# Kernel optimization log

Hardware: AMD Instinct MI355X
Metric: run time of the kernel (lower is better)

## Reference

```python
import jax, jax.numpy as jnp
import numpy as np

LN_EPS = 1e-5


def setup_inputs() -> dict:
    key = jax.random.key(0)
    ks = jax.random.split(key, 8)
    N, c_z, H, C = 256, 128, 4, 32
    s = 0.02  # small init scale for stable softmax
    return {
        "z": jax.random.normal(ks[0], (N, N, c_z), dtype=jnp.float32),
        "ln_g": jnp.ones((c_z,), jnp.float32),
        "ln_b": jnp.zeros((c_z,), jnp.float32),
        "Wb": jax.random.normal(ks[1], (c_z, H), dtype=jnp.float32) * s,
        "Wq": jax.random.normal(ks[2], (c_z, H, C), dtype=jnp.float32) * s,
        "Wk": jax.random.normal(ks[3], (c_z, H, C), dtype=jnp.float32) * s,
        "Wv": jax.random.normal(ks[4], (c_z, H, C), dtype=jnp.float32) * s,
        "Wg": jax.random.normal(ks[5], (c_z, H, C), dtype=jnp.float32) * s,
        "bg": jnp.ones((H, C), jnp.float32),
        "Wo": jax.random.normal(ks[6], (H, C, c_z), dtype=jnp.float32) * s,
        "bo": jnp.zeros((c_z,), jnp.float32),
    }


def reference(z, ln_g, ln_b, Wb, Wq, Wk, Wv, Wg, bg, Wo, bo):
    # TriangleAttention, node_type='starting_node' (Algorithm 13).
    # z: (N, N, c_z)
    C = Wq.shape[-1]
    # LayerNorm over c_z
    mu = jnp.mean(z, axis=-1, keepdims=True)
    var = jnp.var(z, axis=-1, keepdims=True)
    x = (z - mu) * jax.lax.rsqrt(var + LN_EPS) * ln_g + ln_b
    # pairwise additive bias: b[h, j, k] = (x @ Wb)[j, k, h]
    b = jnp.einsum('jkz,zh->hjk', x, Wb)
    # per-head projections; attention over second residue axis (-2),
    # first residue axis i acts as batch
    q = jnp.einsum('ijz,zhc->ijhc', x, Wq)
    k = jnp.einsum('ijz,zhc->ijhc', x, Wk)
    v = jnp.einsum('ijz,zhc->ijhc', x, Wv)
    scores = jnp.einsum('iqhc,ikhc->hiqk', q, k) / jnp.sqrt(jnp.asarray(C, x.dtype))
    scores = scores + b[:, None, :, :]  # broadcast bias over batch axis i
    a = jax.nn.softmax(scores, axis=-1)  # (h, i, q, k)
    o = jnp.einsum('hiqk,ikhc->iqhc', a, v)
    g = jax.nn.sigmoid(jnp.einsum('ijz,zhc->ijhc', x, Wg) + bg)
    o = o * g
    out = jnp.einsum('iqhc,hcz->iqz', o, Wo) + bo
    return out
```

## Files before the change

kernel.cpp:

```cpp
#include <hip/hip_runtime.h>
#include <hip/hip_bf16.h>
#include <math.h>


#define NN 256
#define CZ 128

typedef __attribute__((ext_vector_type(8))) short bf16x8;
typedef __attribute__((ext_vector_type(4))) float f32x4;

__device__ __forceinline__ f32x4 mfma16(bf16x8 a, bf16x8 b, f32x4 c) {
  return __builtin_amdgcn_mfma_f32_16x16x32_bf16(a, b, c, 0, 0, 0);
}
__device__ __forceinline__ unsigned short f2bf(float f) {
  unsigned b = __float_as_uint(f);
  return (unsigned short)((b + 0x7FFFu + ((b >> 16) & 1u)) >> 16);
}

__global__ __launch_bounds__(128) void k_prep(const float* __restrict__ Wq, const float* __restrict__ Wk,
                                              const float* __restrict__ Wv, const float* __restrict__ Wg,
                                              const float* __restrict__ Wo, unsigned short* __restrict__ Wt) {
  int n = blockIdx.x, t = threadIdx.x;
  const float* srcs[5] = {Wq, Wk, Wv, Wg, Wo};
  float v = srcs[n >> 7][t * 128 + (n & 127)];
  Wt[n * 128 + t] = f2bf(v);
}

__global__ __launch_bounds__(256) void k_ln(const float* __restrict__ z,
                                            const float* __restrict__ ln_g,
                                            const float* __restrict__ ln_b,
                                            const float* __restrict__ Wb,
                                            unsigned short* __restrict__ xb,
                                            float* __restrict__ bT) {
  int wave = threadIdx.x >> 6, lane = threadIdx.x & 63;
  int pos = blockIdx.x * 4 + wave;
  float2 v = ((const float2*)(z + (size_t)pos * CZ))[lane];
  float s = v.x + v.y, sq = v.x * v.x + v.y * v.y;
#pragma unroll
  for (int o = 1; o < 64; o <<= 1) { s += __shfl_xor(s, o); sq += __shfl_xor(sq, o); }
  float mean = s * (1.0f / CZ);
  float var = sq * (1.0f / CZ) - mean * mean;
  float rstd = rsqrtf(var + 1e-5f);
  int c0 = lane * 2;
  float x0 = (v.x - mean) * rstd * ln_g[c0] + ln_b[c0];
  float x1 = (v.y - mean) * rstd * ln_g[c0 + 1] + ln_b[c0 + 1];
  unsigned pk = (unsigned)f2bf(x0) | ((unsigned)f2bf(x1) << 16);
  ((unsigned*)(xb + (size_t)pos * CZ))[lane] = pk;
  float4 w0 = *(const float4*)(Wb + c0 * 4);
  float4 w1 = *(const float4*)(Wb + (c0 + 1) * 4);
  float b0 = x0 * w0.x + x1 * w1.x;
  float b1 = x0 * w0.y + x1 * w1.y;
  float b2 = x0 * w0.z + x1 * w1.z;
  float b3 = x0 * w0.w + x1 * w1.w;
#pragma unroll
  for (int o = 1; o < 64; o <<= 1) {
    b0 += __shfl_xor(b0, o); b1 += __shfl_xor(b1, o);
    b2 += __shfl_xor(b2, o); b3 += __shfl_xor(b3, o);
  }
  if (lane == 0) {
    int j = pos >> 8, kk = pos & 255;
    bT[0 * 65536 + kk * 256 + j] = b0;
    bT[1 * 65536 + kk * 256 + j] = b1;
    bT[2 * 65536 + kk * 256 + j] = b2;
    bT[3 * 65536 + kk * 256 + j] = b3;
  }
}

__global__ __launch_bounds__(512, 1) void k_fused(const unsigned short* __restrict__ xb,
                                                  const unsigned short* __restrict__ Wt,
                                                  const float* __restrict__ bT,
                                                  const float* __restrict__ bg,
                                                  const float* __restrict__ bo,
                                                  float* __restrict__ out) {
  __shared__ unsigned short ks[256][40];
  __shared__ unsigned short vt[32][264];
  __shared__ unsigned short qs[8][32][40];
  int i = blockIdx.x;
  int t = threadIdx.x, w = t >> 6, lane = t & 63, l16 = lane & 15, g = lane >> 4;
  int rbase = w * 32;
  const float sc = 0.17677669529663687f;

  bf16x8 xa[2][4];
#pragma unroll
  for (int m = 0; m < 2; m++)
#pragma unroll
    for (int kt = 0; kt < 4; kt++)
      xa[m][kt] = *(const bf16x8*)(xb + (size_t)(i * 256 + rbase + m * 16 + l16) * CZ + kt * 32 + g * 8);

  f32x4 oac[2][8];
#pragma unroll
  for (int m = 0; m < 2; m++)
#pragma unroll
    for (int n = 0; n < 8; n++) oac[m][n] = (f32x4){0.f, 0.f, 0.f, 0.f};

  for (int h = 0; h < 4; h++) {
    __syncthreads();
    f32x4 d[2][2];
#pragma unroll
    for (int m = 0; m < 2; m++)
#pragma unroll
      for (int n = 0; n < 2; n++) d[m][n] = (f32x4){0.f, 0.f, 0.f, 0.f};
#pragma unroll
    for (int kt = 0; kt < 4; kt++)
#pragma unroll
      for (int n = 0; n < 2; n++) {
        bf16x8 b = *(const bf16x8*)(Wt + (size_t)(128 + h * 32 + n * 16 + l16) * CZ + kt * 32 + g * 8);
#pragma unroll
        for (int m = 0; m < 2; m++) d[m][n] = mfma16(xa[m][kt], b, d[m][n]);
      }
#pragma unroll
    for (int m = 0; m < 2; m++)
#pragma unroll
      for (int n = 0; n < 2; n++)
#pragma unroll
        for (int r = 0; r < 4; r++) ks[rbase + m * 16 + g * 4 + r][n * 16 + l16] = f2bf(d[m][n][r]);
#pragma unroll
    for (int m = 0; m < 2; m++)
#pragma unroll
      for (int n = 0; n < 2; n++) d[m][n] = (f32x4){0.f, 0.f, 0.f, 0.f};
#pragma unroll
    for (int kt = 0; kt < 4; kt++)
#pragma unroll
      for (int n = 0; n < 2; n++) {
        bf16x8 b = *(const bf16x8*)(Wt + (size_t)(256 + h * 32 + n * 16 + l16) * CZ + kt * 32 + g * 8);
#pragma unroll
        for (int m = 0; m < 2; m++) d[m][n] = mfma16(xa[m][kt], b, d[m][n]);
      }
#pragma unroll
    for (int m = 0; m < 2; m++)
#pragma unroll
      for (int n = 0; n < 2; n++) {
        ushort4 pk;
        pk.x = f2bf(d[m][n][0]); pk.y = f2bf(d[m][n][1]);
        pk.z = f2bf(d[m][n][2]); pk.w = f2bf(d[m][n][3]);
        *(ushort4*)&vt[n * 16 + l16][rbase + m * 16 + g * 4] = pk;
      }
#pragma unroll
    for (int m = 0; m < 2; m++)
#pragma unroll
      for (int n = 0; n < 2; n++) d[m][n] = (f32x4){0.f, 0.f, 0.f, 0.f};
#pragma unroll
    for (int kt = 0; kt < 4; kt++)
#pragma unroll
      for (int n = 0; n < 2; n++) {
        bf16x8 b = *(const bf16x8*)(Wt + (size_t)(0 + h * 32 + n * 16 + l16) * CZ + kt * 32 + g * 8);
#pragma unroll
        for (int m = 0; m < 2; m++) d[m][n] = mfma16(xa[m][kt], b, d[m][n]);
      }
#pragma unroll
    for (int m = 0; m < 2; m++)
#pragma unroll
      for (int n = 0; n < 2; n++)
#pragma unroll
        for (int r = 0; r < 4; r++) qs[w][m * 16 + g * 4 + r][n * 16 + l16] = f2bf(d[m][n][r]);
#pragma unroll
    for (int m = 0; m < 2; m++)
#pragma unroll
      for (int n = 0; n < 2; n++) d[m][n] = (f32x4){0.f, 0.f, 0.f, 0.f};
#pragma unroll
    for (int kt = 0; kt < 4; kt++)
#pragma unroll
      for (int n = 0; n < 2; n++) {
        bf16x8 b = *(const bf16x8*)(Wt + (size_t)(384 + h * 32 + n * 16 + l16) * CZ + kt * 32 + g * 8);
#pragma unroll
        for (int m = 0; m < 2; m++) d[m][n] = mfma16(xa[m][kt], b, d[m][n]);
      }
    float gt[2][2][4];
    float bgv0 = bg[h * 32 + l16], bgv1 = bg[h * 32 + 16 + l16];
#pragma unroll
    for (int m = 0; m < 2; m++)
#pragma unroll
      for (int n = 0; n < 2; n++)
#pragma unroll
        for (int r = 0; r < 4; r++)
          gt[m][n][r] = 1.0f / (1.0f + __expf(-(d[m][n][r] + (n ? bgv1 : bgv0))));
    __syncthreads();

    bf16x8 qa[2];
#pragma unroll
    for (int m = 0; m < 2; m++) qa[m] = *(const bf16x8*)&qs[w][m * 16 + l16][g * 8];
    f32x4 oat[2][2], lsum[2];
#pragma unroll
    for (int m = 0; m < 2; m++) {
      lsum[m] = (f32x4){0.f, 0.f, 0.f, 0.f};
#pragma unroll
      for (int n = 0; n < 2; n++) oat[m][n] = (f32x4){0.f, 0.f, 0.f, 0.f};
    }
    const float* bb = bT + (size_t)h * 65536;
    for (int kc = 0; kc < 8; kc++) {
      bf16x8 kb[2];
#pragma unroll
      for (int n = 0; n < 2; n++) kb[n] = *(const bf16x8*)&ks[kc * 32 + n * 16 + l16][g * 8];
      f32x4 p[2][2];
#pragma unroll
      for (int m = 0; m < 2; m++)
#pragma unroll
        for (int n = 0; n < 2; n++) {
          f32x4 s = mfma16(qa[m], kb[n], (f32x4){0.f, 0.f, 0.f, 0.f});
          float4 bv = *(const float4*)(bb + (size_t)(kc * 32 + n * 16 + l16) * 256 + rbase + m * 16 + g * 4);
          p[m][n][0] = __expf(s[0] * sc + bv.x);
          p[m][n][1] = __expf(s[1] * sc + bv.y);
          p[m][n][2] = __expf(s[2] * sc + bv.z);
          p[m][n][3] = __expf(s[3] * sc + bv.w);
          lsum[m] += p[m][n];
        }
#pragma unroll
      for (int m = 0; m < 2; m++)
#pragma unroll
        for (int n = 0; n < 2; n++)
#pragma unroll
          for (int r = 0; r < 4; r++) qs[w][m * 16 + g * 4 + r][n * 16 + l16] = f2bf(p[m][n][r]);
      bf16x8 pa[2], vb[2];
#pragma unroll
      for (int m = 0; m < 2; m++) pa[m] = *(const bf16x8*)&qs[w][m * 16 + l16][g * 8];
#pragma unroll
      for (int n = 0; n < 2; n++) vb[n] = *(const bf16x8*)&vt[n * 16 + l16][kc * 32 + g * 8];
#pragma unroll
      for (int m = 0; m < 2; m++)
#pragma unroll
        for (int n = 0; n < 2; n++) oat[m][n] = mfma16(pa[m], vb[n], oat[m][n]);
    }
#pragma unroll
    for (int m = 0; m < 2; m++)
#pragma unroll
      for (int off = 1; off < 16; off <<= 1)
#pragma unroll
        for (int r = 0; r < 4; r++) lsum[m][r] += __shfl_xor(lsum[m][r], off);
#pragma unroll
    for (int m = 0; m < 2; m++) {
      f32x4 inv;
#pragma unroll
      for (int r = 0; r < 4; r++) inv[r] = 1.0f / lsum[m][r];
#pragma unroll
      for (int n = 0; n < 2; n++)
#pragma unroll
        for (int r = 0; r < 4; r++)
          qs[w][m * 16 + g * 4 + r][n * 16 + l16] = f2bf(oat[m][n][r] * inv[r] * gt[m][n][r]);
    }
    bf16x8 pa2[2];
#pragma unroll
    for (int m = 0; m < 2; m++) pa2[m] = *(const bf16x8*)&qs[w][m * 16 + l16][g * 8];
#pragma unroll
    for (int n2 = 0; n2 < 8; n2++) {
      bf16x8 wb = *(const bf16x8*)(Wt + (size_t)(512 + n2 * 16 + l16) * CZ + h * 32 + g * 8);
#pragma unroll
      for (int m = 0; m < 2; m++) oac[m][n2] = mfma16(pa2[m], wb, oac[m][n2]);
    }
  }
#pragma unroll
  for (int n2 = 0; n2 < 8; n2++) {
    int zc = n2 * 16 + l16;
    float bv = bo[zc];
#pragma unroll
    for (int m = 0; m < 2; m++)
#pragma unroll
      for (int r = 0; r < 4; r++)
        out[(size_t)(i * 256 + rbase + m * 16 + g * 4 + r) * 128 + zc] = oac[m][n2][r] + bv;
  }
}

extern "C" void kernel_launch(void* const* d_in, const int* in_sizes, int n_in,
                              void* d_out, int out_size, void* d_ws, size_t ws_size,
                              hipStream_t stream) {
  const float* z    = (const float*)d_in[0];
  const float* ln_g = (const float*)d_in[1];
  const float* ln_b = (const float*)d_in[2];
  const float* Wb   = (const float*)d_in[3];
  const float* Wq   = (const float*)d_in[4];
  const float* Wk   = (const float*)d_in[5];
  const float* Wv   = (const float*)d_in[6];
  const float* Wg   = (const float*)d_in[7];
  const float* bg   = (const float*)d_in[8];
  const float* Wo   = (const float*)d_in[9];
  const float* bo   = (const float*)d_in[10];
  float* out = (float*)d_out;

  char* ws = (char*)d_ws;
  unsigned short* xb = (unsigned short*)(ws + 0);
  float*          bT = (float*)(ws + 16777216);
  unsigned short* Wt = (unsigned short*)(ws + 17825792);

  k_prep<<<640, 128, 0, stream>>>(Wq, Wk, Wv, Wg, Wo, Wt);
  k_ln<<<16384, 256, 0, stream>>>(z, ln_g, ln_b, Wb, xb, bT);
  k_fused<<<256, 512, 0, stream>>>(xb, Wt, bT, bg, bo, out);
}
```

Before: 217.1 us.

## Split fused attention into per-head blocks plus a separate output-projection GEMM

The single fused kernel (one 512-thread block per batch row, looping over 4 heads) is replaced by a per-(row, head) kernel with 256 threads and higher occupancy. Each warp now handles 64 query rows. The gated attention output is written to a bf16 workspace, and a separate k_out GEMM kernel applies Wo and bo. This exposes 4x more blocks to fill the GPU and removes the per-head barrier loop. The cost is an extra global round trip of the gated output, an extra launch, and redundant reads of xb per head.

Measured after the change: 223.2 us. 1.03x slower.

```diff
diff --git a/kernel.cpp b/kernel.cpp
--- a/kernel.cpp
+++ b/kernel.cpp
@@ -66,42 +66,37 @@
   }
 }
 
-__global__ __launch_bounds__(512, 1) void k_fused(const unsigned short* __restrict__ xb,
-                                                  const unsigned short* __restrict__ Wt,
-                                                  const float* __restrict__ bT,
-                                                  const float* __restrict__ bg,
-                                                  const float* __restrict__ bo,
-                                                  float* __restrict__ out) {
+__global__ __launch_bounds__(256, 3) void k_head(const unsigned short* __restrict__ xb,
+                                                 const unsigned short* __restrict__ Wt,
+                                                 const float* __restrict__ bT,
+                                                 const float* __restrict__ bg,
+                                                 unsigned short* __restrict__ og) {
   __shared__ unsigned short ks[256][40];
   __shared__ unsigned short vt[32][264];
-  __shared__ unsigned short qs[8][32][40];
-  int i = blockIdx.x;
+  __shared__ unsigned short qs[4][32][40];
+  int i = blockIdx.x, h = blockIdx.y;
   int t = threadIdx.x, w = t >> 6, lane = t & 63, l16 = lane & 15, g = lane >> 4;
-  int rbase = w * 32;
   const float sc = 0.17677669529663687f;
 
-  bf16x8 xa[2][4];
-#pragma unroll
-  for (int m = 0; m < 2; m++)
+  bf16x8 qa[2][2];
+  f32x4 gt[2][2][2];
+
+#pragma unroll
+  for (int rh = 0; rh < 2; rh++) {
+    int r0 = w * 64 + rh * 32;
+    bf16x8 xa[2][4];
+#pragma unroll
+    for (int m = 0; m < 2; m++)
+#pragma unroll
+      for (int kt = 0; kt < 4; kt++)
+        xa[m][kt] = *(const bf16x8*)(xb + (size_t)(i * 256 + r0 + m * 16 + l16) * CZ + kt * 32 + g * 8);
+    f32x4 d[2][2];
+#pragma unroll
+    for (int m = 0; m < 2; m++)
+#pragma unroll
+      for (int n = 0; n < 2; n++) d[m][n] = (f32x4){0.f, 0.f, 0.f, 0.f};
 #pragma unroll
     for (int kt = 0; kt < 4; kt++)
-      xa[m][kt] = *(const bf16x8*)(xb + (size_t)(i * 256 + rbase + m * 16 + l16) * CZ + kt * 32 + g * 8);
-
-  f32x4 oac[2][8];
-#pragma unroll
-  for (int m = 0; m < 2; m++)
-#pragma unroll
-    for (int n = 0; n < 8; n++) oac[m][n] = (f32x4){0.f, 0.f, 0.f, 0.f};
-
-  for (int h = 0; h < 4; h++) {
-    __syncthreads();
-    f32x4 d[2][2];
-#pragma unroll
-    for (int m = 0; m < 2; m++)
-#pragma unroll
-      for (int n = 0; n < 2; n++) d[m][n] = (f32x4){0.f, 0.f, 0.f, 0.f};
-#pragma unroll
-    for (int kt = 0; kt < 4; kt++)
 #pragma unroll
       for (int n = 0; n < 2; n++) {
         bf16x8 b = *(const bf16x8*)(Wt + (size_t)(128 + h * 32 + n * 16 + l16) * CZ + kt * 32 + g * 8);
@@ -113,7 +108,7 @@
 #pragma unroll
       for (int n = 0; n < 2; n++)
 #pragma unroll
-        for (int r = 0; r < 4; r++) ks[rbase + m * 16 + g * 4 + r][n * 16 + l16] = f2bf(d[m][n][r]);
+        for (int r = 0; r < 4; r++) ks[r0 + m * 16 + g * 4 + r][n * 16 + l16] = f2bf(d[m][n][r]);
 #pragma unroll
     for (int m = 0; m < 2; m++)
 #pragma unroll
@@ -133,7 +128,7 @@
         ushort4 pk;
         pk.x = f2bf(d[m][n][0]); pk.y = f2bf(d[m][n][1]);
         pk.z = f2bf(d[m][n][2]); pk.w = f2bf(d[m][n][3]);
-        *(ushort4*)&vt[n * 16 + l16][rbase + m * 16 + g * 4] = pk;
+        *(ushort4*)&vt[n * 16 + l16][r0 + m * 16 + g * 4] = pk;
       }
 #pragma unroll
     for (int m = 0; m < 2; m++)
@@ -154,6 +149,8 @@
 #pragma unroll
         for (int r = 0; r < 4; r++) qs[w][m * 16 + g * 4 + r][n * 16 + l16] = f2bf(d[m][n][r]);
 #pragma unroll
+    for (int m = 0; m < 2; m++) qa[rh][m] = *(const bf16x8*)&qs[w][m * 16 + l16][g * 8];
+#pragma unroll
     for (int m = 0; m < 2; m++)
 #pragma unroll
       for (int n = 0; n < 2; n++) d[m][n] = (f32x4){0.f, 0.f, 0.f, 0.f};
@@ -165,7 +162,6 @@
 #pragma unroll
         for (int m = 0; m < 2; m++) d[m][n] = mfma16(xa[m][kt], b, d[m][n]);
       }
-    float gt[2][2][4];
     float bgv0 = bg[h * 32 + l16], bgv1 = bg[h * 32 + 16 + l16];
 #pragma unroll
     for (int m = 0; m < 2; m++)
@@ -173,12 +169,14 @@
       for (int n = 0; n < 2; n++)
 #pragma unroll
         for (int r = 0; r < 4; r++)
-          gt[m][n][r] = 1.0f / (1.0f + __expf(-(d[m][n][r] + (n ? bgv1 : bgv0))));
-    __syncthreads();
-
-    bf16x8 qa[2];
-#pragma unroll
-    for (int m = 0; m < 2; m++) qa[m] = *(const bf16x8*)&qs[w][m * 16 + l16][g * 8];
+          gt[rh][m][n][r] = 1.0f / (1.0f + __expf(-(d[m][n][r] + (n ? bgv1 : bgv0))));
+  }
+  __syncthreads();
+
+  const float* bb = bT + (size_t)h * 65536;
+#pragma unroll
+  for (int qh = 0; qh < 2; qh++) {
+    int rq = w * 64 + qh * 32;
     f32x4 oat[2][2], lsum[2];
 #pragma unroll
     for (int m = 0; m < 2; m++) {
@@ -186,7 +184,6 @@
 #pragma unroll
       for (int n = 0; n < 2; n++) oat[m][n] = (f32x4){0.f, 0.f, 0.f, 0.f};
     }
-    const float* bb = bT + (size_t)h * 65536;
     for (int kc = 0; kc < 8; kc++) {
       bf16x8 kb[2];
 #pragma unroll
@@ -196,8 +193,8 @@
       for (int m = 0; m < 2; m++)
 #pragma unroll
         for (int n = 0; n < 2; n++) {
-          f32x4 s = mfma16(qa[m], kb[n], (f32x4){0.f, 0.f, 0.f, 0.f});
-          float4 bv = *(const float4*)(bb + (size_t)(kc * 32 + n * 16 + l16) * 256 + rbase + m * 16 + g * 4);
+          f32x4 s = mfma16(qa[qh][m], kb[n], (f32x4){0.f, 0.f, 0.f, 0.f});
+          float4 bv = *(const float4*)(bb + (size_t)(kc * 32 + n * 16 + l16) * 256 + rq + m * 16 + g * 4);
           p[m][n][0] = __expf(s[0] * sc + bv.x);
           p[m][n][1] = __expf(s[1] * sc + bv.y);
           p[m][n][2] = __expf(s[2] * sc + bv.z);
@@ -235,27 +232,54 @@
       for (int n = 0; n < 2; n++)
 #pragma unroll
         for (int r = 0; r < 4; r++)
-          qs[w][m * 16 + g * 4 + r][n * 16 + l16] = f2bf(oat[m][n][r] * inv[r] * gt[m][n][r]);
-    }
-    bf16x8 pa2[2];
-#pragma unroll
-    for (int m = 0; m < 2; m++) pa2[m] = *(const bf16x8*)&qs[w][m * 16 + l16][g * 8];
-#pragma unroll
-    for (int n2 = 0; n2 < 8; n2++) {
-      bf16x8 wb = *(const bf16x8*)(Wt + (size_t)(512 + n2 * 16 + l16) * CZ + h * 32 + g * 8);
-#pragma unroll
-      for (int m = 0; m < 2; m++) oac[m][n2] = mfma16(pa2[m], wb, oac[m][n2]);
-    }
-  }
-#pragma unroll
-  for (int n2 = 0; n2 < 8; n2++) {
-    int zc = n2 * 16 + l16;
+          qs[w][m * 16 + g * 4 + r][n * 16 + l16] = f2bf(oat[m][n][r] * inv[r] * gt[qh][m][n][r]);
+    }
+#pragma unroll
+    for (int e = 0; e < 4; e++) {
+      int idx = e * 64 + lane;
+      int row = idx >> 3, c4 = (idx & 7) * 4;
+      *(ushort4*)(og + (size_t)(i * 256 + rq + row) * 128 + h * 32 + c4) = *(ushort4*)&qs[w][row][c4];
+    }
+  }
+}
+
+__global__ __launch_bounds__(256) void k_out(const unsigned short* __restrict__ og,
+                                             const unsigned short* __restrict__ WoT,
+                                             const float* __restrict__ bo,
+                                             float* __restrict__ out) {
+  int t = threadIdx.x, w = t >> 6, lane = t & 63, l16 = lane & 15, g = lane >> 4;
+  int wr = w >> 1, wc = w & 1;
+  int pbase = blockIdx.x * 128 + wr * 64;
+  int cbase = wc * 64;
+  f32x4 acc[4][4];
+#pragma unroll
+  for (int m = 0; m < 4; m++)
+#pragma unroll
+    for (int n = 0; n < 4; n++) acc[m][n] = (f32x4){0.f, 0.f, 0.f, 0.f};
+#pragma unroll
+  for (int kt = 0; kt < 4; kt++) {
+    bf16x8 a[4], b[4];
+#pragma unroll
+    for (int m = 0; m < 4; m++)
+      a[m] = *(const bf16x8*)(og + (size_t)(pbase + m * 16 + l16) * 128 + kt * 32 + g * 8);
+#pragma unroll
+    for (int n = 0; n < 4; n++)
+      b[n] = *(const bf16x8*)(WoT + (size_t)(cbase + n * 16 + l16) * 128 + kt * 32 + g * 8);
+#pragma unroll
+    for (int m = 0; m < 4; m++)
+#pragma unroll
+      for (int n = 0; n < 4; n++) acc[m][n] = mfma16(a[m], b[n], acc[m][n]);
+  }
+#pragma unroll
+  for (int n = 0; n < 4; n++) {
+    int zc = cbase + n * 16 + l16;
     float bv = bo[zc];
 #pragma unroll
-    for (int m = 0; m < 2; m++)
+    for (int m = 0; m < 4; m++) {
 #pragma unroll
       for (int r = 0; r < 4; r++)
-        out[(size_t)(i * 256 + rbase + m * 16 + g * 4 + r) * 128 + zc] = oac[m][n2][r] + bv;
+        out[(size_t)(pbase + m * 16 + g * 4 + r) * 128 + zc] = acc[m][n][r] + bv;
+    }
   }
 }
 
@@ -279,8 +303,10 @@
   unsigned short* xb = (unsigned short*)(ws + 0);
   float*          bT = (float*)(ws + 16777216);
   unsigned short* Wt = (unsigned short*)(ws + 17825792);
+  unsigned short* og = (unsigned short*)(ws + 17989632);
 
   k_prep<<<640, 128, 0, stream>>>(Wq, Wk, Wv, Wg, Wo, Wt);
   k_ln<<<16384, 256, 0, stream>>>(z, ln_g, ln_b, Wb, xb, bT);
-  k_fused<<<256, 512, 0, stream>>>(xb, Wt, bT, bg, bo, out);
-}
+  k_head<<<dim3(256, 4), 256, 0, stream>>>(xb, Wt, bT, bg, og);
+  k_out<<<512, 256, 0, stream>>>(og, Wt + 512 * 128, bo, out);
+}
```
